# Optimization experiments

Hardware: AMD Instinct MI355X
Metric: run time of the kernel (lower is better)

The kernel has to match this reference:

```python
import jax, jax.numpy as jnp
import numpy as np

B, D, C, P = 1024, 768, 150, 64  # batch, in_feats, num_labels, proj2 dim
POS_M, NEG_M = 0.7, 1.4


def setup_inputs() -> dict:
    key = jax.random.key(0)
    ks = jax.random.split(key, 8)
    return {
        "x": jax.random.normal(ks[0], (B, D), jnp.float32),
        "lb": jax.random.randint(ks[1], (B,), 0, C + 1),
        "mem": jax.random.normal(ks[2], (C, D), jnp.float32),
        "fc_w": jax.random.normal(ks[3], (2 * D, 2 * D), jnp.float32) * 0.02,
        "fc_b": jnp.zeros((2 * D,), jnp.float32),
        "p1_w": jax.random.normal(ks[4], (1, 2 * D), jnp.float32) * 0.02,
        "p1_b": jnp.zeros((1,), jnp.float32),
        "p2_w": jax.random.normal(ks[5], (P, 2 * D), jnp.float32) * 0.02,
        "p2_b": jnp.zeros((P,), jnp.float32),
    }


def reference(x, lb, mem, fc_w, fc_b, p1_w, p1_b, p2_w, p2_b):
    d = x.shape[1]
    # cat([a, b], 1) @ fc_w.T == a @ Wx.T + b @ Wm.T  (exact split of the linear)
    Wx, Wm = fc_w[:, :d], fc_w[:, d:]
    xh = x @ Wx.T + fc_b                                # [B, 2D]

    # --- get_logit ---
    seen_h = jax.nn.relu(xh[:, None, :] + mem @ Wm.T)   # [B, C, 2D]
    seen = jnp.einsum('bce,e->bc', seen_h, p1_w[0]) + p1_b[0]   # [B, C]
    uh = jax.nn.relu(xh)                                # cat([x, zeros]) path
    unseen = uh @ p1_w.T + p1_b                         # [B, 1]
    logits = jnp.concatenate([seen, unseen], axis=1)    # [B, C+1]

    # --- masked log-softmax losses (pos_adapte) ---
    labels = jax.nn.one_hot(lb, C + 1, dtype=jnp.float32)
    th = jnp.zeros_like(labels).at[:, -1].set(1.0)
    labels = labels.at[:, -1].set(0.0)
    p_mask = labels + th
    n_mask = 1.0 - labels
    BIG = 1e30
    loss1 = -(jax.nn.log_softmax(logits - (1.0 - p_mask) * BIG, -1) * labels).sum(1)
    loss2 = -(jax.nn.log_softmax(logits - (1.0 - n_mask) * BIG, -1) * th).sum(1)
    loss_cls = (loss1 + loss2).mean()

    # --- metric loss on unseen embedding ---
    u = uh @ p2_w.T + p2_b                              # [B, 64]
    u = u / jnp.maximum(jnp.linalg.norm(u, axis=1, keepdims=True), 1e-12)
    sq_n = (u * u).sum(1)
    sq = sq_n[:, None] + sq_n[None, :] - 2.0 * (u @ u.T)
    err = sq <= 0.0
    dist = jnp.sqrt(jnp.clip(sq, 1e-16, None)) * (~err).astype(u.dtype)
    same = lb[:, None] == lb[None, :]
    eye = jnp.eye(dist.shape[0], dtype=bool)
    pos = (same & ~eye).astype(dist.dtype)
    neg = (~same).astype(dist.dtype)
    pos_l = (jax.nn.relu(dist - POS_M) * pos).sum() / jnp.maximum(pos.sum(), 1.0)
    neg_l = (jax.nn.relu(NEG_M - dist) * neg).sum() / jnp.maximum(neg.sum(), 1.0)

    return loss_cls + pos_l + neg_l
```

## Files before the change

### kernel.cpp

```cpp
#include <hip/hip_runtime.h>
#include <math.h>

#define B_    1024
#define D_    768
#define C_    150
#define P_    64
#define TWOD  1536
#define NCLS  151
#define CPAD  256

#define ECHUNKS 16
#define ECHUNK  96

#define ASTR  40
#define USTRU 120
#define USTR  72

#define OFF_MH      0
#define OFF_XH      (OFF_MH + (C_ * TWOD) / 2)
#define OFF_PARTIAL (OFF_XH + (B_ * TWOD) / 2)
#define OFF_UHF     (OFF_PARTIAL + ECHUNKS * B_ * CPAD)
#define OFF_SQN     (OFF_UHF + (B_ * P_) / 2)
#define OFF_CLS     (OFF_SQN + B_)
#define OFF_PAIR    (OFF_CLS + B_)
#define OFF_XBF     (OFF_PAIR + 1024)
#define OFF_MEMBF   (OFF_XBF + (B_ * D_) / 2)
#define OFF_WBF     (OFF_MEMBF + (C_ * D_) / 2)
#define OFF_P2H     (OFF_WBF + (TWOD * TWOD) / 2)
#define OFF_P1H     (OFF_P2H + (P_ * TWOD) / 2)

typedef __bf16    bfx8   __attribute__((ext_vector_type(8)));
typedef _Float16  fp16x8 __attribute__((ext_vector_type(8)));
typedef _Float16  h2v    __attribute__((ext_vector_type(2)));
typedef float     f32x4  __attribute__((ext_vector_type(4)));

__device__ inline ushort f2bf(float f) {
    union { float f; unsigned u; } c; c.f = f;
    unsigned r = c.u + 0x7fffu + ((c.u >> 16) & 1u);
    return (ushort)(r >> 16);
}
__device__ inline ushort f2h(float f) {
    _Float16 h = (_Float16)f;
    return __builtin_bit_cast(ushort, h);
}
__device__ inline unsigned addrelu2(unsigned a, unsigned m) {
    h2v s = __builtin_bit_cast(h2v, a) + __builtin_bit_cast(h2v, m);
    h2v z = {(_Float16)0.f, (_Float16)0.f};
    s = __builtin_elementwise_max(s, z);
    return __builtin_bit_cast(unsigned, s);
}
__device__ inline unsigned relu2(unsigned a) {
    h2v s = __builtin_bit_cast(h2v, a);
    h2v z = {(_Float16)0.f, (_Float16)0.f};
    s = __builtin_elementwise_max(s, z);
    return __builtin_bit_cast(unsigned, s);
}
__device__ inline float dot2acc(unsigned a, unsigned b, float c) {
    return __builtin_amdgcn_fdot2(__builtin_bit_cast(h2v, a),
                                  __builtin_bit_cast(h2v, b), c, false);
}

#define X4   (B_ * D_ / 4)
#define MEM4 (C_ * D_ / 4)
#define W4   (TWOD * TWOD / 4)
#define P24  (P_ * TWOD / 4)
#define P14  (TWOD / 4)
#define TOT4 (X4 + MEM4 + W4 + P24 + P14)

__global__ __launch_bounds__(256) void prep_cvt(
    const float* __restrict__ x, const float* __restrict__ mem,
    const float* __restrict__ w, const float* __restrict__ p2w,
    const float* __restrict__ p1w,
    ushort* __restrict__ xb, ushort* __restrict__ memb,
    ushort* __restrict__ wb, ushort* __restrict__ p2h,
    ushort* __restrict__ p1h)
{
    int i = blockIdx.x * 256 + threadIdx.x;
    if (i >= TOT4) return;
    const float* src; ushort* dst; int off; bool bf;
    if (i < X4)                        { src = x;   dst = xb;   off = i; bf = true; }
    else if (i < X4 + MEM4)            { src = mem; dst = memb; off = i - X4; bf = true; }
    else if (i < X4 + MEM4 + W4)       { src = w;   dst = wb;   off = i - X4 - MEM4; bf = true; }
    else if (i < X4 + MEM4 + W4 + P24) { src = p2w; dst = p2h;  off = i - X4 - MEM4 - W4; bf = false; }
    else                               { src = p1w; dst = p1h;  off = i - X4 - MEM4 - W4 - P24; bf = false; }
    float4 v = ((const float4*)src)[off];
    ushort4 o;
    if (bf) { o.x = f2bf(v.x); o.y = f2bf(v.y); o.z = f2bf(v.z); o.w = f2bf(v.w); }
    else    { o.x = f2h(v.x);  o.y = f2h(v.y);  o.z = f2h(v.z);  o.w = f2h(v.w); }
    ((ushort4*)dst)[off] = o;
}

__global__ __launch_bounds__(256) void gemm_all(
    const ushort* __restrict__ xbf, const ushort* __restrict__ membf,
    const ushort* __restrict__ wbf, const float* __restrict__ fc_b,
    ushort* __restrict__ xh, ushort* __restrict__ mh)
{
    __shared__ ushort As[64 * ASTR];
    __shared__ ushort Bs[128 * ASTR];
    const int id = blockIdx.x;
    const int t  = threadIdx.x;

    const ushort* A; ushort* Out; int M, m0, n0, koff; bool xblk;
    if (id < 192) {
        xblk = true;  A = xbf;  Out = xh; M = B_;
        m0 = (id & 15) * 64; n0 = (id >> 4) * 128; koff = 0;
    } else {
        int q = id - 192;
        xblk = false; A = membf; Out = mh; M = C_;
        m0 = (q % 3) * 64; n0 = (q / 3) * 128; koff = D_;
    }

    const int wave = t >> 6, lane = t & 63;
    const int wm = (wave & 1) * 32, wn = (wave >> 1) * 64;
    const int fm = lane & 15, quad = lane >> 4;

    const int row_a = t >> 2, qa = (t & 3) * 8;
    const int ar = min(m0 + row_a, M - 1);
    const ushort* Arow = A + (size_t)ar * D_ + qa;
    const ushort* Brow = wbf + (size_t)(n0 + row_a) * TWOD + koff + qa;

    f32x4 acc[2][4];
#pragma unroll
    for (int j = 0; j < 4; ++j) {
        float bv = xblk ? fc_b[n0 + wn + j * 16 + fm] : 0.f;
#pragma unroll
        for (int i = 0; i < 2; ++i)
            acc[i][j] = (f32x4){bv, bv, bv, bv};
    }

    uint4 pa  = *(const uint4*)(Arow);
    uint4 pb0 = *(const uint4*)(Brow);
    uint4 pb1 = *(const uint4*)(Brow + 64 * TWOD);

    for (int k0 = 0; k0 < D_; k0 += 32) {
        __syncthreads();
        *(uint4*)&As[row_a * ASTR + qa] = pa;
        *(uint4*)&Bs[row_a * ASTR + qa] = pb0;
        *(uint4*)&Bs[(64 + row_a) * ASTR + qa] = pb1;
        __syncthreads();
        if (k0 + 32 < D_) {
            pa  = *(const uint4*)(Arow + k0 + 32);
            pb0 = *(const uint4*)(Brow + k0 + 32);
            pb1 = *(const uint4*)(Brow + 64 * TWOD + k0 + 32);
        }
        bfx8 af[2], bf[4];
#pragma unroll
        for (int i = 0; i < 2; ++i)
            af[i] = *(const bfx8*)&As[(wm + i * 16 + fm) * ASTR + quad * 8];
#pragma unroll
        for (int j = 0; j < 4; ++j)
            bf[j] = *(const bfx8*)&Bs[(wn + j * 16 + fm) * ASTR + quad * 8];
#pragma unroll
        for (int i = 0; i < 2; ++i)
#pragma unroll
            for (int j = 0; j < 4; ++j)
                acc[i][j] = __builtin_amdgcn_mfma_f32_16x16x32_bf16(
                    af[i], bf[j], acc[i][j], 0, 0, 0);
    }

#pragma unroll
    for (int i = 0; i < 2; ++i)
#pragma unroll
        for (int j = 0; j < 4; ++j)
#pragma unroll
            for (int r = 0; r < 4; ++r) {
                int row = m0 + wm + i * 16 + quad * 4 + r;
                int col = n0 + wn + j * 16 + fm;
                if (row < M) Out[(size_t)row * TWOD + col] = f2h(acc[i][j][r]);
            }
}

__global__ __launch_bounds__(256) void fused_tile(
    const ushort* __restrict__ xh, const ushort* __restrict__ mh,
    const ushort* __restrict__ p1h, const ushort* __restrict__ p2h,
    float* __restrict__ partial)
{
    __shared__ __align__(16) char smem[46080];
    const int t  = threadIdx.x;
    const int b0 = blockIdx.x * 128;
    const int z  = blockIdx.z;
    const int e0 = z * ECHUNK;

    if (blockIdx.y == 3) {
        ushort* Au = (ushort*)smem;
        ushort* Wu = (ushort*)(smem + 30720);
        const int wave = t >> 6, lane = t & 63;
        const int fm = lane & 15, quad = lane >> 4;

        {
            const int row = t >> 1, kh = (t & 1) * 48;
            const ushort* src = xh + (size_t)(b0 + row) * TWOD + e0 + kh;
            uint4 v[6];
#pragma unroll
            for (int i = 0; i < 6; ++i) v[i] = *(const uint4*)&src[i * 8];
#pragma unroll
            for (int i = 0; i < 6; ++i) {
                v[i].x = relu2(v[i].x); v[i].y = relu2(v[i].y);
                v[i].z = relu2(v[i].z); v[i].w = relu2(v[i].w);
                *(uint4*)&Au[row * USTRU + kh + i * 8] = v[i];
            }
        }
        {
            const int row = t >> 2, ks = (t & 3) * 24;
            const ushort* pw = p2h + (size_t)row * TWOD + e0 + ks;
#pragma unroll
            for (int i = 0; i < 3; ++i)
                *(uint4*)&Wu[row * USTRU + ks + i * 8] = *(const uint4*)&pw[i * 8];
        }
        __syncthreads();

        f32x4 uacc[2][4];
#pragma unroll
        for (int i = 0; i < 2; ++i)
#pragma unroll
            for (int j = 0; j < 4; ++j) uacc[i][j] = (f32x4){0.f, 0.f, 0.f, 0.f};
#pragma unroll
        for (int k0 = 0; k0 < ECHUNK; k0 += 32) {
            fp16x8 af[2], bf[4];
#pragma unroll
            for (int i = 0; i < 2; ++i)
                af[i] = *(const fp16x8*)&Au[(wave * 32 + i * 16 + fm) * USTRU + k0 + quad * 8];
#pragma unroll
            for (int j = 0; j < 4; ++j)
                bf[j] = *(const fp16x8*)&Wu[(j * 16 + fm) * USTRU + k0 + quad * 8];
#pragma unroll
            for (int i = 0; i < 2; ++i)
#pragma unroll
                for (int j = 0; j < 4; ++j)
                    uacc[i][j] = __builtin_amdgcn_mfma_f32_16x16x32_f16(
                        af[i], bf[j], uacc[i][j], 0, 0, 0);
        }
#pragma unroll
        for (int i = 0; i < 2; ++i)
#pragma unroll
            for (int j = 0; j < 4; ++j)
#pragma unroll
                for (int r = 0; r < 4; ++r) {
                    int row = b0 + wave * 32 + i * 16 + quad * 4 + r;
                    partial[((size_t)z * B_ + row) * CPAD + 192 + j * 16 + fm] =
                        uacc[i][j][r];
                }
        return;
    }

    unsigned* xT = (unsigned*)smem;
    unsigned* mT = (unsigned*)(smem + 24576);
    unsigned* wT = (unsigned*)(smem + 36864);
    const int c0 = blockIdx.y * 64;
    const int tm = t & 15, tn = t >> 4;

    {
        const int row = t >> 1, ph = (t & 1) * 48;
        const ushort* src = xh + (size_t)(b0 + row) * TWOD + e0 + ph;
        uint4 v[6];
#pragma unroll
        for (int i = 0; i < 6; ++i) v[i] = *(const uint4*)&src[i * 8];
#pragma unroll
        for (int i = 0; i < 6; ++i) {
            const int ep = (t & 1) * 24 + i * 4;
            xT[(ep + 0) * 128 + row] = v[i].x;
            xT[(ep + 1) * 128 + row] = v[i].y;
            xT[(ep + 2) * 128 + row] = v[i].z;
            xT[(ep + 3) * 128 + row] = v[i].w;
        }
    }
    {
        const int col = t & 63, seg = t >> 6;
        const int gc  = c0 + col;
        uint4 v[3];
        if (gc < C_) {
            const ushort* src = mh + (size_t)gc * TWOD + e0 + seg * 24;
#pragma unroll
            for (int i = 0; i < 3; ++i) v[i] = *(const uint4*)&src[i * 8];
        } else {
#pragma unroll
            for (int i = 0; i < 3; ++i) v[i] = make_uint4(0, 0, 0, 0);
        }
#pragma unroll
        for (int i = 0; i < 3; ++i) {
            const int ep = seg * 12 + i * 4;
            mT[(ep + 0) * 64 + col] = v[i].x;
            mT[(ep + 1) * 64 + col] = v[i].y;
            mT[(ep + 2) * 64 + col] = v[i].z;
            mT[(ep + 3) * 64 + col] = v[i].w;
        }
    }
    if (t < 12) {
        uint4 v = *(const uint4*)&p1h[e0 + t * 8];
        wT[t * 4 + 0] = v.x; wT[t * 4 + 1] = v.y;
        wT[t * 4 + 2] = v.z; wT[t * 4 + 3] = v.w;
    }
    __syncthreads();

    float acc[8][4] = {};
#pragma unroll 4
    for (int ep = 0; ep < 48; ++ep) {
        uint4 a0 = *(const uint4*)&xT[ep * 128 + tm * 8];
        uint4 a1 = *(const uint4*)&xT[ep * 128 + tm * 8 + 4];
        uint4 mj = *(const uint4*)&mT[ep * 64 + tn * 4];
        const unsigned wv = wT[ep];
        const unsigned aa[8] = {a0.x, a0.y, a0.z, a0.w, a1.x, a1.y, a1.z, a1.w};
        const unsigned mm[4] = {mj.x, mj.y, mj.z, mj.w};
#pragma unroll
        for (int i = 0; i < 8; ++i)
#pragma unroll
            for (int j = 0; j < 4; ++j)
                acc[i][j] = dot2acc(addrelu2(aa[i], mm[j]), wv, acc[i][j]);
    }

#pragma unroll
    for (int i = 0; i < 8; ++i) {
        const int gb = b0 + tm * 8 + i;
        float4 v = make_float4(acc[i][0], acc[i][1], acc[i][2], acc[i][3]);
        *(float4*)&partial[((size_t)z * B_ + gb) * CPAD + c0 + tn * 4] = v;
    }
}

__global__ __launch_bounds__(256) void reduce_row(
    const float* __restrict__ partial,
    const float* __restrict__ p1b, const float* __restrict__ p2b,
    const int* __restrict__ lb,
    ushort* __restrict__ uhf, float* __restrict__ sqn,
    float* __restrict__ clsbuf)
{
    const int b = blockIdx.x, t = threadIdx.x;
    float v = 0.f;
#pragma unroll
    for (int z = 0; z < ECHUNKS; ++z)
        v += partial[((size_t)z * B_ + b) * CPAD + t];
    if (t < NCLS)       v += p1b[0];
    else if (t >= 192)  v += p2b[t - 192];

    __shared__ float sval[256];
    sval[t] = v;
    __syncthreads();

    if (t < 64) {
        float uv = sval[192 + t];
        float s = uv * uv;
#pragma unroll
        for (int off = 32; off; off >>= 1) s += __shfl_xor(s, off);
        float inv = 1.f / fmaxf(sqrtf(s), 1e-12f);
        uhf[(size_t)b * P_ + t] = f2h(uv * inv);
        if (t == 0) sqn[b] = s * inv * inv;

        const int l = lb[b];
        float mx = -1e30f;
        for (int j = t; j < NCLS; j += 64)
            if (!(j == l && l < C_)) mx = fmaxf(mx, sval[j]);
#pragma unroll
        for (int off = 32; off; off >>= 1) mx = fmaxf(mx, __shfl_xor(mx, off));
        float se = 0.f;
        for (int j = t; j < NCLS; j += 64)
            if (!(j == l && l < C_)) se += expf(sval[j] - mx);
#pragma unroll
        for (int off = 32; off; off >>= 1) se += __shfl_xor(se, off);

        if (t == 0) {
            float l150  = sval[C_];
            float loss2 = mx + logf(se) - l150;
            float loss1 = 0.f;
            if (l < C_) {
                float a  = sval[l];
                float m2 = fmaxf(a, l150);
                loss1 = m2 - a + logf(expf(a - m2) + expf(l150 - m2));
            }
            clsbuf[b] = loss1 + loss2;
        }
    }
}

__global__ __launch_bounds__(256) void pair_loss(
    const ushort* __restrict__ uhf, const float* __restrict__ sqn,
    const int* __restrict__ lb, float* __restrict__ pairpart)
{
    __shared__ ushort ui_s[64 * USTR];
    __shared__ ushort uj_s[64 * USTR];
    __shared__ float sni[64], snj[64];
    __shared__ int   li[64],  lj[64];
    __shared__ float red[4][4];

    const int t  = threadIdx.x;
    const int i0 = blockIdx.x * 64, j0 = blockIdx.y * 64;

    for (int idx = t; idx < 512; idx += 256) {
        int row = idx >> 3, ch = (idx & 7) * 8;
        *(uint4*)&ui_s[row * USTR + ch] =
            *(const uint4*)&uhf[(size_t)(i0 + row) * P_ + ch];
        *(uint4*)&uj_s[row * USTR + ch] =
            *(const uint4*)&uhf[(size_t)(j0 + row) * P_ + ch];
    }
    if (t < 64)       { sni[t] = sqn[i0 + t]; li[t] = lb[i0 + t]; }
    else if (t < 128) { int q = t - 64; snj[q] = sqn[j0 + q]; lj[q] = lb[j0 + q]; }
    __syncthreads();

    const int wave = t >> 6, lane = t & 63;
    const int n = lane & 15, quad = lane >> 4;
    const int iw = wave * 16;

    const fp16x8 af0 = *(const fp16x8*)&ui_s[(iw + n) * USTR + quad * 8];
    const fp16x8 af1 = *(const fp16x8*)&ui_s[(iw + n) * USTR + quad * 8 + 32];

    f32x4 acc[4];
#pragma unroll
    for (int jt = 0; jt < 4; ++jt) {
        const fp16x8 bf0 = *(const fp16x8*)&uj_s[(jt * 16 + n) * USTR + quad * 8];
        const fp16x8 bf1 = *(const fp16x8*)&uj_s[(jt * 16 + n) * USTR + quad * 8 + 32];
        acc[jt] = __builtin_amdgcn_mfma_f32_16x16x32_f16(
            af0, bf0, (f32x4){0.f, 0.f, 0.f, 0.f}, 0, 0, 0);
        acc[jt] = __builtin_amdgcn_mfma_f32_16x16x32_f16(
            af1, bf1, acc[jt], 0, 0, 0);
    }

    float ps = 0.f, pc = 0.f, ns = 0.f, nc = 0.f;
#pragma unroll
    for (int jt = 0; jt < 4; ++jt)
#pragma unroll
        for (int r = 0; r < 4; ++r) {
            const int il = iw + quad * 4 + r;
            const int jl = jt * 16 + n;
            float sq = sni[il] + snj[jl] - 2.f * acc[jt][r];
            float dist = sq > 0.f ? sqrtf(fmaxf(sq, 1e-16f)) : 0.f;
            bool same = (li[il] == lj[jl]);
            if (same) {
                if (i0 + il != j0 + jl) { ps += fmaxf(dist - 0.7f, 0.f); pc += 1.f; }
            } else {
                ns += fmaxf(1.4f - dist, 0.f); nc += 1.f;
            }
        }

#pragma unroll
    for (int off = 32; off; off >>= 1) {
        ps += __shfl_xor(ps, off); pc += __shfl_xor(pc, off);
        ns += __shfl_xor(ns, off); nc += __shfl_xor(nc, off);
    }
    if (lane == 0) { red[0][wave] = ps; red[1][wave] = pc;
                     red[2][wave] = ns; red[3][wave] = nc; }
    __syncthreads();
    if (t == 0) {
        float4 v;
        v.x = red[0][0] + red[0][1] + red[0][2] + red[0][3];
        v.y = red[1][0] + red[1][1] + red[1][2] + red[1][3];
        v.z = red[2][0] + red[2][1] + red[2][2] + red[2][3];
        v.w = red[3][0] + red[3][1] + red[3][2] + red[3][3];
        *(float4*)&pairpart[(size_t)(blockIdx.y * 16 + blockIdx.x) * 4] = v;
    }
}

__global__ __launch_bounds__(256) void finalize(
    const float* __restrict__ clsbuf, const float* __restrict__ pairpart,
    float* __restrict__ out)
{
    __shared__ float red[5][4];
    const int t = threadIdx.x;
    float c = clsbuf[t] + clsbuf[t + 256] + clsbuf[t + 512] + clsbuf[t + 768];
    float4 pp = *(const float4*)&pairpart[(size_t)t * 4];
    float ps = pp.x, pc = pp.y, ns = pp.z, nc = pp.w;
#pragma unroll
    for (int off = 32; off; off >>= 1) {
        c  += __shfl_xor(c, off);
        ps += __shfl_xor(ps, off); pc += __shfl_xor(pc, off);
        ns += __shfl_xor(ns, off); nc += __shfl_xor(nc, off);
    }
    const int wave = t >> 6, lane = t & 63;
    if (lane == 0) { red[0][wave] = c; red[1][wave] = ps; red[2][wave] = pc;
                     red[3][wave] = ns; red[4][wave] = nc; }
    __syncthreads();
    if (t == 0) {
        float C = 0.f, PS = 0.f, PC = 0.f, NS = 0.f, NC = 0.f;
#pragma unroll
        for (int w = 0; w < 4; ++w) {
            C += red[0][w]; PS += red[1][w]; PC += red[2][w];
            NS += red[3][w]; NC += red[4][w];
        }
        out[0] = C / (float)B_ + PS / fmaxf(PC, 1.f) + NS / fmaxf(NC, 1.f);
    }
}

extern "C" void kernel_launch(void* const* d_in, const int* in_sizes, int n_in,
                              void* d_out, int out_size, void* d_ws, size_t ws_size,
                              hipStream_t stream)
{
    const float* x    = (const float*)d_in[0];
    const int*   lb   = (const int*)d_in[1];
    const float* mem  = (const float*)d_in[2];
    const float* fc_w = (const float*)d_in[3];
    const float* fc_b = (const float*)d_in[4];
    const float* p1w  = (const float*)d_in[5];
    const float* p1b  = (const float*)d_in[6];
    const float* p2w  = (const float*)d_in[7];
    const float* p2b  = (const float*)d_in[8];

    float* ws       = (float*)d_ws;
    ushort* mh      = (ushort*)(ws + OFF_MH);
    ushort* xh      = (ushort*)(ws + OFF_XH);
    float* partials = ws + OFF_PARTIAL;
    ushort* uhf     = (ushort*)(ws + OFF_UHF);
    float* sqn      = ws + OFF_SQN;
    float* clsbuf   = ws + OFF_CLS;
    float* pairpart = ws + OFF_PAIR;
    ushort* xbf     = (ushort*)(ws + OFF_XBF);
    ushort* membf   = (ushort*)(ws + OFF_MEMBF);
    ushort* wbf     = (ushort*)(ws + OFF_WBF);
    ushort* p2h     = (ushort*)(ws + OFF_P2H);
    ushort* p1h     = (ushort*)(ws + OFF_P1H);

    prep_cvt<<<(TOT4 + 255) / 256, 256, 0, stream>>>(x, mem, fc_w, p2w, p1w,
                                                     xbf, membf, wbf, p2h, p1h);
    gemm_all<<<228, 256, 0, stream>>>(xbf, membf, wbf, fc_b, xh, mh);
    fused_tile<<<dim3(8, 4, ECHUNKS), 256, 0, stream>>>(xh, mh, p1h, p2h,
                                                        partials);
    reduce_row<<<B_, 256, 0, stream>>>(partials, p1b, p2b, lb, uhf, sqn, clsbuf);
    pair_loss<<<dim3(16, 16), 256, 0, stream>>>(uhf, sqn, lb, pairpart);
    finalize<<<1, 256, 0, stream>>>(clsbuf, pairpart, (float*)d_out);
}
```

Baseline: 132.2 us.

## Fuse fp32-to-bf16 conversion into GEMM and finalize into pair_loss

Drops the separate prep_cvt pass. The GEMM now loads fp32 x, mem and fc_w directly and converts them to bf16 in registers before staging into LDS, and 13 extra blocks convert the small p1/p2 weights to fp16. The finalize kernel is merged into pair_loss through an atomic counter, so the last block does the final reduction. This removes two launches and a full write and read of the converted fc_w, x and mem arrays, at the cost of doubled global load bytes per GEMM tile and redundant conversion of fc_w across M-tiles.

```diff
diff --git a/kernel.cpp b/kernel.cpp
--- a/kernel.cpp
+++ b/kernel.cpp
@@ -23,10 +23,8 @@
 #define OFF_SQN     (OFF_UHF + (B_ * P_) / 2)
 #define OFF_CLS     (OFF_SQN + B_)
 #define OFF_PAIR    (OFF_CLS + B_)
-#define OFF_XBF     (OFF_PAIR + 1024)
-#define OFF_MEMBF   (OFF_XBF + (B_ * D_) / 2)
-#define OFF_WBF     (OFF_MEMBF + (C_ * D_) / 2)
-#define OFF_P2H     (OFF_WBF + (TWOD * TWOD) / 2)
+#define OFF_CTR     (OFF_PAIR + 1024)
+#define OFF_P2H     (OFF_CTR + 4)
 #define OFF_P1H     (OFF_P2H + (P_ * TWOD) / 2)
 
 typedef __bf16    bfx8   __attribute__((ext_vector_type(8)));
@@ -59,54 +57,52 @@
     return __builtin_amdgcn_fdot2(__builtin_bit_cast(h2v, a),
                                   __builtin_bit_cast(h2v, b), c, false);
 }
-
-#define X4   (B_ * D_ / 4)
-#define MEM4 (C_ * D_ / 4)
-#define W4   (TWOD * TWOD / 4)
+__device__ inline uint4 cvt8bf(float4 a, float4 b) {
+    ushort o[8];
+    o[0] = f2bf(a.x); o[1] = f2bf(a.y); o[2] = f2bf(a.z); o[3] = f2bf(a.w);
+    o[4] = f2bf(b.x); o[5] = f2bf(b.y); o[6] = f2bf(b.z); o[7] = f2bf(b.w);
+    return *(const uint4*)&o[0];
+}
+
 #define P24  (P_ * TWOD / 4)
 #define P14  (TWOD / 4)
-#define TOT4 (X4 + MEM4 + W4 + P24 + P14)
-
-__global__ __launch_bounds__(256) void prep_cvt(
-    const float* __restrict__ x, const float* __restrict__ mem,
-    const float* __restrict__ w, const float* __restrict__ p2w,
-    const float* __restrict__ p1w,
-    ushort* __restrict__ xb, ushort* __restrict__ memb,
-    ushort* __restrict__ wb, ushort* __restrict__ p2h,
-    ushort* __restrict__ p1h)
+
+__global__ __launch_bounds__(256) void gemm_all(
+    const float* __restrict__ xf, const float* __restrict__ memf,
+    const float* __restrict__ fcw, const float* __restrict__ fc_b,
+    const float* __restrict__ p2w, const float* __restrict__ p1w,
+    ushort* __restrict__ xh, ushort* __restrict__ mh,
+    ushort* __restrict__ p2h, ushort* __restrict__ p1h,
+    int* __restrict__ ctr)
 {
-    int i = blockIdx.x * 256 + threadIdx.x;
-    if (i >= TOT4) return;
-    const float* src; ushort* dst; int off; bool bf;
-    if (i < X4)                        { src = x;   dst = xb;   off = i; bf = true; }
-    else if (i < X4 + MEM4)            { src = mem; dst = memb; off = i - X4; bf = true; }
-    else if (i < X4 + MEM4 + W4)       { src = w;   dst = wb;   off = i - X4 - MEM4; bf = true; }
-    else if (i < X4 + MEM4 + W4 + P24) { src = p2w; dst = p2h;  off = i - X4 - MEM4 - W4; bf = false; }
-    else                               { src = p1w; dst = p1h;  off = i - X4 - MEM4 - W4 - P24; bf = false; }
-    float4 v = ((const float4*)src)[off];
-    ushort4 o;
-    if (bf) { o.x = f2bf(v.x); o.y = f2bf(v.y); o.z = f2bf(v.z); o.w = f2bf(v.w); }
-    else    { o.x = f2h(v.x);  o.y = f2h(v.y);  o.z = f2h(v.z);  o.w = f2h(v.w); }
-    ((ushort4*)dst)[off] = o;
-}
-
-__global__ __launch_bounds__(256) void gemm_all(
-    const ushort* __restrict__ xbf, const ushort* __restrict__ membf,
-    const ushort* __restrict__ wbf, const float* __restrict__ fc_b,
-    ushort* __restrict__ xh, ushort* __restrict__ mh)
-{
+    const int id = blockIdx.x;
+    const int t  = threadIdx.x;
+
+    if (id >= 228) {
+        if (id == 228 && t == 0) *ctr = 0;
+        const int cid = id - 228;
+        for (int i = cid * 256 + t; i < P24 + P14; i += 13 * 256) {
+            const float* src; ushort* dst; int off;
+            if (i < P24) { src = p2w; dst = p2h; off = i; }
+            else         { src = p1w; dst = p1h; off = i - P24; }
+            float4 v = ((const float4*)src)[off];
+            ushort4 o;
+            o.x = f2h(v.x); o.y = f2h(v.y); o.z = f2h(v.z); o.w = f2h(v.w);
+            ((ushort4*)dst)[off] = o;
+        }
+        return;
+    }
+
     __shared__ ushort As[64 * ASTR];
     __shared__ ushort Bs[128 * ASTR];
-    const int id = blockIdx.x;
-    const int t  = threadIdx.x;
-
-    const ushort* A; ushort* Out; int M, m0, n0, koff; bool xblk;
+
+    const float* A; ushort* Out; int M, m0, n0, koff; bool xblk;
     if (id < 192) {
-        xblk = true;  A = xbf;  Out = xh; M = B_;
+        xblk = true;  A = xf;   Out = xh; M = B_;
         m0 = (id & 15) * 64; n0 = (id >> 4) * 128; koff = 0;
     } else {
         int q = id - 192;
-        xblk = false; A = membf; Out = mh; M = C_;
+        xblk = false; A = memf; Out = mh; M = C_;
         m0 = (q % 3) * 64; n0 = (q / 3) * 128; koff = D_;
     }
 
@@ -116,8 +112,9 @@
 
     const int row_a = t >> 2, qa = (t & 3) * 8;
     const int ar = min(m0 + row_a, M - 1);
-    const ushort* Arow = A + (size_t)ar * D_ + qa;
-    const ushort* Brow = wbf + (size_t)(n0 + row_a) * TWOD + koff + qa;
+    const float* Arow  = A + (size_t)ar * D_ + qa;
+    const float* Brow0 = fcw + (size_t)(n0 + row_a) * TWOD + koff + qa;
+    const float* Brow1 = Brow0 + (size_t)64 * TWOD;
 
     f32x4 acc[2][4];
 #pragma unroll
@@ -128,20 +125,26 @@
             acc[i][j] = (f32x4){bv, bv, bv, bv};
     }
 
-    uint4 pa  = *(const uint4*)(Arow);
-    uint4 pb0 = *(const uint4*)(Brow);
-    uint4 pb1 = *(const uint4*)(Brow + 64 * TWOD);
+    float4 pa0  = *(const float4*)(Arow),   pa1  = *(const float4*)(Arow + 4);
+    float4 pb00 = *(const float4*)(Brow0),  pb01 = *(const float4*)(Brow0 + 4);
+    float4 pb10 = *(const float4*)(Brow1),  pb11 = *(const float4*)(Brow1 + 4);
 
     for (int k0 = 0; k0 < D_; k0 += 32) {
+        uint4 va  = cvt8bf(pa0, pa1);
+        uint4 vb0 = cvt8bf(pb00, pb01);
+        uint4 vb1 = cvt8bf(pb10, pb11);
         __syncthreads();
-        *(uint4*)&As[row_a * ASTR + qa] = pa;
-        *(uint4*)&Bs[row_a * ASTR + qa] = pb0;
-        *(uint4*)&Bs[(64 + row_a) * ASTR + qa] = pb1;
+        *(uint4*)&As[row_a * ASTR + qa] = va;
+        *(uint4*)&Bs[row_a * ASTR + qa] = vb0;
+        *(uint4*)&Bs[(64 + row_a) * ASTR + qa] = vb1;
         __syncthreads();
         if (k0 + 32 < D_) {
-            pa  = *(const uint4*)(Arow + k0 + 32);
-            pb0 = *(const uint4*)(Brow + k0 + 32);
-            pb1 = *(const uint4*)(Brow + 64 * TWOD + k0 + 32);
+            pa0  = *(const float4*)(Arow + k0 + 32);
+            pa1  = *(const float4*)(Arow + k0 + 36);
+            pb00 = *(const float4*)(Brow0 + k0 + 32);
+            pb01 = *(const float4*)(Brow0 + k0 + 36);
+            pb10 = *(const float4*)(Brow1 + k0 + 32);
+            pb11 = *(const float4*)(Brow1 + k0 + 36);
         }
         bfx8 af[2], bf[4];
 #pragma unroll
@@ -372,16 +375,20 @@
 
 __global__ __launch_bounds__(256) void pair_loss(
     const ushort* __restrict__ uhf, const float* __restrict__ sqn,
-    const int* __restrict__ lb, float* __restrict__ pairpart)
+    const int* __restrict__ lb, const float* __restrict__ clsbuf,
+    float* __restrict__ pairpart, int* __restrict__ ctr,
+    float* __restrict__ out)
 {
     __shared__ ushort ui_s[64 * USTR];
     __shared__ ushort uj_s[64 * USTR];
     __shared__ float sni[64], snj[64];
     __shared__ int   li[64],  lj[64];
-    __shared__ float red[4][4];
+    __shared__ float red[5][4];
+    __shared__ int   isLast;
 
     const int t  = threadIdx.x;
-    const int i0 = blockIdx.x * 64, j0 = blockIdx.y * 64;
+    const int id = blockIdx.x;
+    const int i0 = (id & 15) * 64, j0 = (id >> 4) * 64;
 
     for (int idx = t; idx < 512; idx += 256) {
         int row = idx >> 3, ch = (idx & 7) * 8;
@@ -443,37 +450,38 @@
         v.y = red[1][0] + red[1][1] + red[1][2] + red[1][3];
         v.z = red[2][0] + red[2][1] + red[2][2] + red[2][3];
         v.w = red[3][0] + red[3][1] + red[3][2] + red[3][3];
-        *(float4*)&pairpart[(size_t)(blockIdx.y * 16 + blockIdx.x) * 4] = v;
-    }
-}
-
-__global__ __launch_bounds__(256) void finalize(
-    const float* __restrict__ clsbuf, const float* __restrict__ pairpart,
-    float* __restrict__ out)
-{
-    __shared__ float red[5][4];
-    const int t = threadIdx.x;
-    float c = clsbuf[t] + clsbuf[t + 256] + clsbuf[t + 512] + clsbuf[t + 768];
-    float4 pp = *(const float4*)&pairpart[(size_t)t * 4];
-    float ps = pp.x, pc = pp.y, ns = pp.z, nc = pp.w;
-#pragma unroll
-    for (int off = 32; off; off >>= 1) {
-        c  += __shfl_xor(c, off);
-        ps += __shfl_xor(ps, off); pc += __shfl_xor(pc, off);
-        ns += __shfl_xor(ns, off); nc += __shfl_xor(nc, off);
-    }
-    const int wave = t >> 6, lane = t & 63;
-    if (lane == 0) { red[0][wave] = c; red[1][wave] = ps; red[2][wave] = pc;
-                     red[3][wave] = ns; red[4][wave] = nc; }
+        *(float4*)&pairpart[(size_t)id * 4] = v;
+        __threadfence();
+        int old = atomicAdd(ctr, 1);
+        isLast = (old == 255);
+    }
     __syncthreads();
-    if (t == 0) {
-        float C = 0.f, PS = 0.f, PC = 0.f, NS = 0.f, NC = 0.f;
-#pragma unroll
-        for (int w = 0; w < 4; ++w) {
-            C += red[0][w]; PS += red[1][w]; PC += red[2][w];
-            NS += red[3][w]; NC += red[4][w];
-        }
-        out[0] = C / (float)B_ + PS / fmaxf(PC, 1.f) + NS / fmaxf(NC, 1.f);
+
+    if (isLast) {
+        __threadfence();
+        float c = clsbuf[t] + clsbuf[t + 256] + clsbuf[t + 512] + clsbuf[t + 768];
+        float4 pp = *(const float4*)&pairpart[(size_t)t * 4];
+        float fps = pp.x, fpc = pp.y, fns = pp.z, fnc = pp.w;
+#pragma unroll
+        for (int off = 32; off; off >>= 1) {
+            c   += __shfl_xor(c, off);
+            fps += __shfl_xor(fps, off); fpc += __shfl_xor(fpc, off);
+            fns += __shfl_xor(fns, off); fnc += __shfl_xor(fnc, off);
+        }
+        __syncthreads();
+        if (lane == 0) { red[0][wave] = c;   red[1][wave] = fps;
+                         red[2][wave] = fpc; red[3][wave] = fns;
+                         red[4][wave] = fnc; }
+        __syncthreads();
+        if (t == 0) {
+            float C = 0.f, PS = 0.f, PC = 0.f, NS = 0.f, NC = 0.f;
+#pragma unroll
+            for (int w = 0; w < 4; ++w) {
+                C += red[0][w]; PS += red[1][w]; PC += red[2][w];
+                NS += red[3][w]; NC += red[4][w];
+            }
+            out[0] = C / (float)B_ + PS / fmaxf(PC, 1.f) + NS / fmaxf(NC, 1.f);
+        }
     }
 }
 
@@ -499,18 +507,15 @@
     float* sqn      = ws + OFF_SQN;
     float* clsbuf   = ws + OFF_CLS;
     float* pairpart = ws + OFF_PAIR;
-    ushort* xbf     = (ushort*)(ws + OFF_XBF);
-    ushort* membf   = (ushort*)(ws + OFF_MEMBF);
-    ushort* wbf     = (ushort*)(ws + OFF_WBF);
+    int*   ctr      = (int*)(ws + OFF_CTR);
     ushort* p2h     = (ushort*)(ws + OFF_P2H);
     ushort* p1h     = (ushort*)(ws + OFF_P1H);
 
-    prep_cvt<<<(TOT4 + 255) / 256, 256, 0, stream>>>(x, mem, fc_w, p2w, p1w,
-                                                     xbf, membf, wbf, p2h, p1h);
-    gemm_all<<<228, 256, 0, stream>>>(xbf, membf, wbf, fc_b, xh, mh);
+    gemm_all<<<241, 256, 0, stream>>>(x, mem, fc_w, fc_b, p2w, p1w,
+                                      xh, mh, p2h, p1h, ctr);
     fused_tile<<<dim3(8, 4, ECHUNKS), 256, 0, stream>>>(xh, mh, p1h, p2h,
                                                         partials);
     reduce_row<<<B_, 256, 0, stream>>>(partials, p1b, p2b, lb, uhf, sqn, clsbuf);
-    pair_loss<<<dim3(16, 16), 256, 0, stream>>>(uhf, sqn, lb, pairpart);
-    finalize<<<1, 256, 0, stream>>>(clsbuf, pairpart, (float*)d_out);
-}
+    pair_loss<<<256, 256, 0, stream>>>(uhf, sqn, lb, clsbuf, pairpart, ctr,
+                                       (float*)d_out);
+}
```

New measurement: 139.8 us. 5.8% more time.
